# Kernel optimization log

Measured on AMD Instinct MI355X. Metric: run time of the kernel, lower is better.

Reference implementation:

```python
import jax, jax.numpy as jnp
import numpy as np
from jax import lax

B, S, V, E, H, L, LAT = 32, 64, 32000, 128, 512, 2, 64

def setup_inputs() -> dict:
    key = jax.random.key(0)
    ks = jax.random.split(key, 40)
    sc = 0.05
    inputs = jax.random.randint(ks[0], (B, S), 0, V, dtype=jnp.int32)
    lengths = jnp.sort(jax.random.randint(ks[1], (B,), 1, S + 1, dtype=jnp.int32))[::-1]
    lengths = lengths.at[0].set(S)  # enforce_sorted=True, max length == S for static shapes
    d = {
        'inputs': inputs,
        'lengths': lengths,
        'noise': jax.random.normal(ks[2], (L, B, LAT), jnp.float32),
        'embed_table': jax.random.normal(ks[3], (V, E), jnp.float32) * sc,
        'enc_Wm': jax.random.normal(ks[4], (LAT, E), jnp.float32) * sc,
        'enc_bm': jnp.zeros((LAT,), jnp.float32),
        'enc_Wv': jax.random.normal(ks[5], (LAT, E), jnp.float32) * sc,
        'enc_bv': jnp.zeros((LAT,), jnp.float32),
        'W_l2r': jax.random.normal(ks[6], (H, LAT), jnp.float32) * sc,
        'b_l2r': jnp.zeros((H,), jnp.float32),
        'gru_Wih0': jax.random.normal(ks[7], (3 * H, E), jnp.float32) * sc,
        'gru_Whh0': jax.random.normal(ks[8], (3 * H, H), jnp.float32) * sc,
        'gru_bih0': jnp.zeros((3 * H,), jnp.float32),
        'gru_bhh0': jnp.zeros((3 * H,), jnp.float32),
        'gru_Wih1': jax.random.normal(ks[9], (3 * H, H), jnp.float32) * sc,
        'gru_Whh1': jax.random.normal(ks[10], (3 * H, H), jnp.float32) * sc,
        'gru_bih1': jnp.zeros((3 * H,), jnp.float32),
        'gru_bhh1': jnp.zeros((3 * H,), jnp.float32),
        'W_out': jax.random.normal(ks[11], (V, H), jnp.float32) * sc,
        'b_out': jnp.zeros((V,), jnp.float32),
        'logp_W1': jax.random.normal(ks[12], (200, LAT), jnp.float32) * sc,
        'logp_b1': jnp.zeros((200,), jnp.float32),
        'logp_W2': jax.random.normal(ks[13], (100, 200), jnp.float32) * sc,
        'logp_b2': jnp.zeros((100,), jnp.float32),
        'logp_W3': jax.random.normal(ks[14], (1, 100), jnp.float32) * sc,
        'logp_b3': jnp.zeros((1,), jnp.float32),
        'sas_W1': jax.random.normal(ks[15], (200, LAT), jnp.float32) * sc,
        'sas_b1': jnp.zeros((200,), jnp.float32),
        'sas_W2': jax.random.normal(ks[16], (100, 200), jnp.float32) * sc,
        'sas_b2': jnp.zeros((100,), jnp.float32),
        'sas_W3': jax.random.normal(ks[17], (1, 100), jnp.float32) * sc,
        'sas_b3': jnp.zeros((1,), jnp.float32),
    }
    return d

def _gru_layer(x, h0, Wih, Whh, bih, bhh, lengths):
    # x: [B,T,D]; PyTorch GRU gate order: r, z, n. Packed semantics: state frozen
    # and output zero beyond each sample's length.
    T = x.shape[1]
    xW = jnp.einsum('btd,gd->btg', x, Wih) + bih          # [B,T,3H] one big GEMM
    tmask = jnp.arange(T)[:, None] < lengths[None, :]      # [T,B]
    def step(h, inp):
        xw_t, m_t = inp                                    # [B,3H], [B]
        hW = h @ Whh.T + bhh
        xr, xz, xn = jnp.split(xw_t, 3, axis=-1)
        hr, hz, hn = jnp.split(hW, 3, axis=-1)
        r = jax.nn.sigmoid(xr + hr)
        u = jax.nn.sigmoid(xz + hz)
        n = jnp.tanh(xn + r * hn)
        h_new = (1.0 - u) * n + u * h
        m = m_t[:, None]
        h = jnp.where(m, h_new, h)
        out = jnp.where(m, h_new, 0.0)
        return h, out
    hT, outs = lax.scan(step, h0, (xW.transpose(1, 0, 2), tmask))
    return outs.transpose(1, 0, 2), hT                     # [B,T,H], [B,H]

def _mlp3(x, W1, b1, W2, b2, W3, b3):
    h = jax.nn.relu(x @ W1.T + b1)
    h = jax.nn.relu(h @ W2.T + b2)
    return (h @ W3.T + b3).reshape(-1)

def reference(inputs, lengths, noise, embed_table, enc_Wm, enc_bm, enc_Wv, enc_bv,
              W_l2r, b_l2r, gru_Wih0, gru_Whh0, gru_bih0, gru_bhh0,
              gru_Wih1, gru_Whh1, gru_bih1, gru_bhh1, W_out, b_out,
              logp_W1, logp_b1, logp_W2, logp_b2, logp_W3, logp_b3,
              sas_W1, sas_b1, sas_W2, sas_b2, sas_W3, sas_b3):
    emb = embed_table[inputs]                              # [B,S,E] gather
    # ragged masked segment-sum: sum embeddings of tokens with id > 2 per sample
    mask = (inputs > 2)[..., None].astype(emb.dtype)
    vec_frag = jnp.sum(emb * mask, axis=1)                 # [B,E]
    mean = vec_frag @ enc_Wm.T + enc_bm                    # [B,LAT]
    logv = vec_frag @ enc_Wv.T + enc_bv
    std = jnp.exp(0.5 * logv)
    z = noise * std + mean                                 # [L,B,LAT]
    pred_logp = _mlp3(mean, logp_W1, logp_b1, logp_W2, logp_b2, logp_W3, logp_b3)
    pred_sas = _mlp3(mean, sas_W1, sas_b1, sas_W2, sas_b2, sas_W3, sas_b3)
    state = z @ W_l2r.T + b_l2r                            # [L,B,H]
    # decoder: 2-layer GRU (eval mode: no dropout), then vocab projection
    out0, _ = _gru_layer(emb, state[0], gru_Wih0, gru_Whh0, gru_bih0, gru_bhh0, lengths)
    out1, _ = _gru_layer(out0, state[1], gru_Wih1, gru_Whh1, gru_bih1, gru_bhh1, lengths)
    output = out1 @ W_out.T + b_out                        # [B,S,V]
    return (output, mean, std, z, pred_logp, pred_sas)
```

## Files before the change

kernel.cpp:

```cpp
#include <hip/hip_runtime.h>


typedef __attribute__((ext_vector_type(8))) short bf16x8_t;
typedef __attribute__((ext_vector_type(8))) unsigned short u16x8_t;
typedef __attribute__((ext_vector_type(4))) float f32x4_t;
typedef __attribute__((ext_vector_type(8))) _Float16 f16x8_t;
typedef __attribute__((ext_vector_type(4))) unsigned int u32x4_t;

#define AS_AGENT __HIP_MEMORY_SCOPE_AGENT

static __device__ __forceinline__ unsigned short f2bf(float f) {
    unsigned int u = __float_as_uint(f);
    u += 0x7fffu + ((u >> 16) & 1u);
    return (unsigned short)(u >> 16);
}
static __device__ __forceinline__ unsigned short f2h(float f) {
    _Float16 h = (_Float16)f;
    return __builtin_bit_cast(unsigned short, h);
}
static __device__ __forceinline__ float sigmoidf_(float x) {
    return 1.f / (1.f + __expf(-x));
}

__global__ __launch_bounds__(256) void embed_encoder_kernel(
    const int* __restrict__ tok, const float* __restrict__ table,
    const float* __restrict__ Wih0f,
    const float* __restrict__ Wm, const float* __restrict__ bm,
    const float* __restrict__ Wv, const float* __restrict__ bv,
    const float* __restrict__ noise,
    const float* __restrict__ Wl2r, const float* __restrict__ bl2r,
    const float* __restrict__ lW1, const float* __restrict__ lb1,
    const float* __restrict__ lW2, const float* __restrict__ lb2,
    const float* __restrict__ lW3, const float* __restrict__ lb3,
    const float* __restrict__ sW1, const float* __restrict__ sb1,
    const float* __restrict__ sW2, const float* __restrict__ sb2,
    const float* __restrict__ sW3, const float* __restrict__ sb3,
    float* __restrict__ o_mean, float* __restrict__ o_std, float* __restrict__ o_z,
    float* __restrict__ o_logp, float* __restrict__ o_sas,
    float* __restrict__ state,
    unsigned short* __restrict__ embb,
    unsigned short* __restrict__ Wih0b)
{
    const int b = blockIdx.x, tid = threadIdx.x;
    __shared__ float v_[128], mn[64], sd[64], zz[2][64], hh1[200], hh2[100];
    if (tid < 128) {
        const int e = tid;
        float acc = 0.f;
        for (int s = 0; s < 64; ++s) {
            int id = tok[b * 64 + s];
            float v = table[(size_t)id * 128 + e];
            embb[(size_t)(b * 64 + s) * 128 + e] = f2bf(v);
            if (id > 2) acc += v;
        }
        v_[e] = acc;
    }
    for (int i = b * 256 + tid; i < 49152; i += 8192) {
        float4 v = reinterpret_cast<const float4*>(Wih0f)[i];
        ushort4 o;
        o.x = f2bf(v.x); o.y = f2bf(v.y); o.z = f2bf(v.z); o.w = f2bf(v.w);
        reinterpret_cast<ushort4*>(Wih0b)[i] = o;
    }
    __syncthreads();
    if (tid < 128) {
        int j = tid & 63;
        bool isv = tid >= 64;
        const float* W = (isv ? Wv : Wm) + j * 128;
        float a = isv ? bv[j] : bm[j];
#pragma unroll 4
        for (int k = 0; k < 128; ++k) a = fmaf(v_[k], W[k], a);
        if (!isv) { mn[j] = a; o_mean[b * 64 + j] = a; }
        else      { float s = __expf(0.5f * a); sd[j] = s; o_std[b * 64 + j] = s; }
    }
    __syncthreads();
    if (tid < 128) {
        int l = tid >> 6, j = tid & 63;
        float zv = fmaf(noise[(l * 32 + b) * 64 + j], sd[j], mn[j]);
        zz[l][j] = zv;
        o_z[(l * 32 + b) * 64 + j] = zv;
    }
    __syncthreads();
#pragma unroll
    for (int p = 0; p < 4; ++p) {
        int tt = p * 256 + tid;
        int l = tt >> 9, hd = tt & 511;
        const float* W = Wl2r + hd * 64;
        float a = bl2r[hd];
#pragma unroll 4
        for (int k = 0; k < 64; ++k) a = fmaf(zz[l][k], W[k], a);
        state[(size_t)(l * 32 + b) * 512 + hd] = a;
    }
    if (tid < 200) {
        const float* W = lW1 + tid * 64;
        float a = lb1[tid];
        for (int k = 0; k < 64; ++k) a = fmaf(mn[k], W[k], a);
        hh1[tid] = fmaxf(a, 0.f);
    }
    __syncthreads();
    if (tid < 100) {
        const float* W = lW2 + tid * 200;
        float a = lb2[tid];
        for (int k = 0; k < 200; ++k) a = fmaf(hh1[k], W[k], a);
        hh2[tid] = fmaxf(a, 0.f);
    }
    __syncthreads();
    if (tid == 0) {
        float a = lb3[0];
        for (int k = 0; k < 100; ++k) a = fmaf(hh2[k], lW3[k], a);
        o_logp[b] = a;
    }
    __syncthreads();
    if (tid < 200) {
        const float* W = sW1 + tid * 64;
        float a = sb1[tid];
        for (int k = 0; k < 64; ++k) a = fmaf(mn[k], W[k], a);
        hh1[tid] = fmaxf(a, 0.f);
    }
    __syncthreads();
    if (tid < 100) {
        const float* W = sW2 + tid * 200;
        float a = sb2[tid];
        for (int k = 0; k < 200; ++k) a = fmaf(hh1[k], W[k], a);
        hh2[tid] = fmaxf(a, 0.f);
    }
    __syncthreads();
    if (tid == 0) {
        float a = sb3[0];
        for (int k = 0; k < 100; ++k) a = fmaf(hh2[k], sW3[k], a);
        o_sas[b] = a;
    }
}

__global__ __launch_bounds__(256) void gemm_bt_kernel(
    const unsigned short* __restrict__ A,
    const unsigned short* __restrict__ B,
    const float* __restrict__ bias,
    float* __restrict__ C,
    int M, int N, int K)
{
    __shared__ unsigned short lA[128 * 64];
    __shared__ unsigned short lB[128 * 64];
    const int tid = threadIdx.x;
    const int lane = tid & 63;
    const int wave = tid >> 6;
    const int wm = wave >> 1, wn = wave & 1;
    const int m0 = blockIdx.y * 128, n0 = blockIdx.x * 128;

    f32x4_t acc[4][4];
#pragma unroll
    for (int i = 0; i < 4; ++i)
#pragma unroll
        for (int j = 0; j < 4; ++j) acc[i][j] = (f32x4_t){0.f, 0.f, 0.f, 0.f};

    for (int kt = 0; kt < K; kt += 64) {
#pragma unroll
        for (int p = 0; p < 4; ++p) {
            int g = p * 256 + tid;
            int row = g >> 3, c8 = g & 7;
            int dst = row * 64 + ((c8 ^ (row & 7)) << 3);
            *(u16x8_t*)&lA[dst] = *(const u16x8_t*)(A + (size_t)(m0 + row) * K + kt + (c8 << 3));
            *(u16x8_t*)&lB[dst] = *(const u16x8_t*)(B + (size_t)(n0 + row) * K + kt + (c8 << 3));
        }
        __syncthreads();
#pragma unroll
        for (int kc = 0; kc < 2; ++kc) {
            bf16x8_t af[4], bfr[4];
            int c8 = kc * 4 + (lane >> 4);
#pragma unroll
            for (int i = 0; i < 4; ++i) {
                int ra = wm * 64 + i * 16 + (lane & 15);
                af[i] = *(const bf16x8_t*)&lA[ra * 64 + ((c8 ^ (ra & 7)) << 3)];
                int rb = wn * 64 + i * 16 + (lane & 15);
                bfr[i] = *(const bf16x8_t*)&lB[rb * 64 + ((c8 ^ (rb & 7)) << 3)];
            }
#pragma unroll
            for (int i = 0; i < 4; ++i)
#pragma unroll
                for (int j = 0; j < 4; ++j)
                    acc[i][j] = __builtin_amdgcn_mfma_f32_16x16x32_bf16(af[i], bfr[j], acc[i][j], 0, 0, 0);
        }
        __syncthreads();
    }
    const int lm = (lane >> 4) * 4, ln = lane & 15;
#pragma unroll
    for (int i = 0; i < 4; ++i) {
        int gm = m0 + wm * 64 + i * 16 + lm;
#pragma unroll
        for (int j = 0; j < 4; ++j) {
            int gn = n0 + wn * 64 + j * 16 + ln;
            float bb = bias ? bias[gn] : 0.f;
#pragma unroll
            for (int r = 0; r < 4; ++r)
                C[(size_t)(gm + r) * N + gn] = acc[i][j][r] + bb;
        }
    }
}

#define NWG_L0 16
#define NWG_TOT 48
#define NWG_ALL 256
#define NWG_GEMM 208
#define OCH 32832

__global__ __launch_bounds__(512) void gru_fused_kernel(
    const float* __restrict__ xW0,
    const float* __restrict__ Whh0, const float* __restrict__ bhh0,
    const float* __restrict__ Whh1, const float* __restrict__ Wih1,
    const float* __restrict__ bih1, const float* __restrict__ bhh1,
    const float* __restrict__ hinit,
    const int* __restrict__ lengths,
    unsigned short* __restrict__ h0x,
    unsigned short* __restrict__ h1x,
    unsigned short* __restrict__ o0x,
    unsigned short* __restrict__ out1x,
    const float* __restrict__ Woutf,
    unsigned short* __restrict__ Woutb,
    const float* __restrict__ bout,
    float* __restrict__ outp,
    int* __restrict__ flags)
{
    __shared__ __align__(16) char smem[157184];
    const int tid = threadIdx.x;
    const int wg = blockIdx.x;
    const int lane = tid & 63;
    const int wave = tid >> 6;
    unsigned int* __restrict__ h0x32 = (unsigned int*)h0x;
    unsigned int* __restrict__ h1x32 = (unsigned int*)h1x;
    unsigned int* __restrict__ o0x32 = (unsigned int*)o0x;
    unsigned int* __restrict__ o1x32 = (unsigned int*)out1x;

    (void)__hip_atomic_load(&flags[0], __ATOMIC_ACQUIRE, AS_AGENT);

    if (wg >= NWG_TOT) {
        unsigned short* lA = (unsigned short*)smem;
        unsigned short* lB = (unsigned short*)(smem + 16384);
        const int g = wg - NWG_TOT;
        const int wm = wave >> 2;
        const int wn = wave & 3;

        for (int i = g * 512 + tid; i < 4096000; i += NWG_GEMM * 512) {
            float4 v = reinterpret_cast<const float4*>(Woutf)[i];
            unsigned int lo = (unsigned int)f2bf(v.x) | ((unsigned int)f2bf(v.y) << 16);
            unsigned int hi = (unsigned int)f2bf(v.z) | ((unsigned int)f2bf(v.w) << 16);
            unsigned long long w = (unsigned long long)lo | ((unsigned long long)hi << 32);
            __hip_atomic_store((unsigned long long*)Woutb + i, w, __ATOMIC_RELAXED, AS_AGENT);
        }
        asm volatile("s_waitcnt vmcnt(0)" ::: "memory");
        __syncthreads();
        if (tid == 0) __hip_atomic_store(&flags[wg << 5], 1, __ATOMIC_RELAXED, AS_AGENT);
        if (wave == 0) {
            for (;;) {
                int mn = 1;
#pragma unroll
                for (int j = 0; j < 4; ++j) {
                    int idx = lane * 4 + j;
                    if (idx < NWG_GEMM) {
                        int v = __hip_atomic_load(&flags[(NWG_TOT + idx) << 5],
                                                  __ATOMIC_RELAXED, AS_AGENT);
                        mn = v < mn ? v : mn;
                    }
                }
                if (__all(mn >= 1)) break;
                __builtin_amdgcn_s_sleep(8);
            }
        }
        __syncthreads();

        int mPrev = -1;
        for (int T = g; T < 4000; T += NWG_GEMM) {
            const int m = T / 250, n = T % 250;
            if (m != mPrev) {
                if (wave == 0) {
                    const int tgt = 4 * m + 6;
                    for (;;) {
                        int v = 0x40000000;
                        if (lane < 32)
                            v = __hip_atomic_load(&flags[(NWG_L0 + lane) << 5],
                                                  __ATOMIC_RELAXED, AS_AGENT);
                        if (__all(v >= tgt)) break;
                        __builtin_amdgcn_s_sleep(8);
                    }
                }
                __syncthreads();
                mPrev = m;
            }
            f32x4_t acc[4][2];
#pragma unroll
            for (int i = 0; i < 4; ++i)
#pragma unroll
                for (int j = 0; j < 2; ++j) acc[i][j] = (f32x4_t){0.f, 0.f, 0.f, 0.f};

            for (int kt = 0; kt < 512; kt += 64) {
#pragma unroll
                for (int p = 0; p < 2; ++p) {
                    int gi = p * 512 + tid;
                    int row = gi >> 3, c8 = gi & 7;
                    int dst = row * 64 + ((c8 ^ (row & 7)) << 3);
                    u32x4_t qa = *(const u32x4_t*)(out1x + (size_t)m * 65664 +
                                                   row * 512 + kt + (c8 << 3));
                    u32x4_t qb = *(const u32x4_t*)(Woutb + ((size_t)(n * 128 + row)) * 512 +
                                                   kt + (c8 << 3));
                    *(u32x4_t*)&lA[dst] = qa;
                    *(u32x4_t*)&lB[dst] = qb;
                }
                __syncthreads();
#pragma unroll
                for (int kc = 0; kc < 2; ++kc) {
                    bf16x8_t af[4], bfr[2];
                    int c8 = kc * 4 + (lane >> 4);
#pragma unroll
                    for (int i = 0; i < 4; ++i) {
                        int ra = wm * 64 + i * 16 + (lane & 15);
                        af[i] = *(const bf16x8_t*)&lA[ra * 64 + ((c8 ^ (ra & 7)) << 3)];
                    }
#pragma unroll
                    for (int j = 0; j < 2; ++j) {
                        int rb = wn * 32 + j * 16 + (lane & 15);
                        bfr[j] = *(const bf16x8_t*)&lB[rb * 64 + ((c8 ^ (rb & 7)) << 3)];
                    }
#pragma unroll
                    for (int i = 0; i < 4; ++i)
#pragma unroll
                        for (int j = 0; j < 2; ++j)
                            acc[i][j] = __builtin_amdgcn_mfma_f32_16x16x32_bf16(
                                af[i], bfr[j], acc[i][j], 0, 0, 0);
                }
                __syncthreads();
            }
            const int lm = (lane >> 4) * 4, ln = lane & 15;
#pragma unroll
            for (int i = 0; i < 4; ++i) {
                int rl0 = wm * 64 + i * 16 + lm;
#pragma unroll
                for (int j = 0; j < 2; ++j) {
                    int gn = n * 128 + wn * 32 + j * 16 + ln;
                    float bb = bout[gn];
#pragma unroll
                    for (int r = 0; r < 4; ++r) {
                        int rl = rl0 + r;
                        int t = 4 * m + (rl >> 5), b = rl & 31;
                        outp[(size_t)(b * 64 + t) * 32000 + gn] = acc[i][j][r] + bb;
                    }
                }
            }
        }
        return;
    }

    unsigned short* Wl = (unsigned short*)smem;
    u32x4_t* hstage4 = (u32x4_t*)(smem + 98304);
    float* csm = (float*)(smem + 131072);
#define CSM(p, gt, b, c) csm[((((p)*3 + (gt)) * 32 + (b)) * 34) + (c)]
    const int gate = wave >> 1;
    const int mt = wave & 1;

    if (wg < NWG_L0) {
        const int d0 = wg * 32;
        for (int idx = tid; idx < 6144; idx += 512) {
            int ln = idx & 63, kk = (idx >> 6) & 15, nt = (idx >> 10) & 1, g_ = idx >> 11;
            int grow = g_ * 512 + d0 + nt * 16 + (ln & 15);
            int k = kk * 32 + ((ln >> 4) << 3);
            const float* src = Whh0 + (size_t)grow * 512 + k;
            f16x8_t v;
#pragma unroll
            for (int j = 0; j < 8; ++j) v[j] = (_Float16)src[j];
            *(f16x8_t*)&Wl[idx << 3] = v;
        }
        const int ub = tid >> 4, dpl = (tid & 15) * 2, ud = d0 + dpl;
        float h_lo = hinit[(size_t)ub * 512 + ud];
        float h_hi = hinit[(size_t)ub * 512 + ud + 1];
        const float br_lo = bhh0[ud],        br_hi = bhh0[ud + 1];
        const float bz_lo = bhh0[512 + ud],  bz_hi = bhh0[512 + ud + 1];
        const float bn_lo = bhh0[1024 + ud], bn_hi = bhh0[1024 + ud + 1];
        const int lenb = lengths[ub];
        {
            unsigned int hw = (unsigned int)f2h(h_lo) | ((unsigned int)f2h(h_hi) << 16);
            __hip_atomic_store(&h0x32[ub * 256 + (ud >> 1)], hw, __ATOMIC_RELAXED, AS_AGENT);
        }
        asm volatile("s_waitcnt vmcnt(0)" ::: "memory");
        __syncthreads();
        if (tid == 0) __hip_atomic_store(&flags[wg << 5], 1, __ATOMIC_RELAXED, AS_AGENT);
        const float* xrow = xW0 + (size_t)(ub * 64) * 1536 + ud;
        float2 px_r = *(const float2*)(xrow);
        float2 px_z = *(const float2*)(xrow + 512);
        float2 px_n = *(const float2*)(xrow + 1024);

        for (int r = 0; r < 64; ++r) {
            if (wave == 0) {
                const int tgt = r + 1;
                for (;;) {
                    int v = 0x40000000;
                    if (lane < NWG_TOT)
                        v = __hip_atomic_load(&flags[lane << 5], __ATOMIC_RELAXED, AS_AGENT);
                    if (__all(v >= tgt)) break;
                    __builtin_amdgcn_s_sleep(1);
                }
            }
            __syncthreads();
            {
                const char* srcb = (const char*)h0x + ((r & 1) << 15);
                u32x4_t q0, q1, q2, q3;
                asm volatile("global_load_dwordx4 %0, %1, off sc0 sc1"
                             : "=v"(q0) : "v"(srcb + ((size_t)tid << 4)) : "memory");
                asm volatile("global_load_dwordx4 %0, %1, off sc0 sc1"
                             : "=v"(q1) : "v"(srcb + ((size_t)(512 + tid) << 4)) : "memory");
                asm volatile("global_load_dwordx4 %0, %1, off sc0 sc1"
                             : "=v"(q2) : "v"(srcb + ((size_t)(1024 + tid) << 4)) : "memory");
                asm volatile("global_load_dwordx4 %0, %1, off sc0 sc1"
                             : "=v"(q3) : "v"(srcb + ((size_t)(1536 + tid) << 4)) : "memory");
                asm volatile("s_waitcnt vmcnt(0)" ::: "memory");
                int g0 = tid, g1 = 512 + tid, g2 = 1024 + tid, g3 = 1536 + tid;
                hstage4[g0 ^ ((g0 >> 6) & 7)] = q0;
                hstage4[g1 ^ ((g1 >> 6) & 7)] = q1;
                hstage4[g2 ^ ((g2 >> 6) & 7)] = q2;
                hstage4[g3 ^ ((g3 >> 6) & 7)] = q3;
            }
            __syncthreads();
            if (wave < 6) {
                const int brow = mt * 16 + (lane & 15);
                const int ko = lane >> 4;
                f32x4_t acc0 = (f32x4_t){0.f, 0.f, 0.f, 0.f};
                f32x4_t acc1 = (f32x4_t){0.f, 0.f, 0.f, 0.f};
#pragma unroll
                for (int kk = 0; kk < 16; ++kk) {
                    int gg = brow * 64 + kk * 4 + ko;
                    f16x8_t af = __builtin_bit_cast(f16x8_t, hstage4[gg ^ (brow & 7)]);
                    f16x8_t bf0 = *(const f16x8_t*)&Wl[(((gate * 2 + 0) * 16 + kk) * 64 + lane) << 3];
                    f16x8_t bf1 = *(const f16x8_t*)&Wl[(((gate * 2 + 1) * 16 + kk) * 64 + lane) << 3];
                    acc0 = __builtin_amdgcn_mfma_f32_16x16x32_f16(af, bf0, acc0, 0, 0, 0);
                    acc1 = __builtin_amdgcn_mfma_f32_16x16x32_f16(af, bf1, acc1, 0, 0, 0);
                }
                const int crow = mt * 16 + ((lane >> 4) << 2), ccol = lane & 15;
#pragma unroll
                for (int rr = 0; rr < 4; ++rr) {
                    CSM(0, gate, crow + rr, ccol) = acc0[rr];
                    CSM(0, gate, crow + rr, 16 + ccol) = acc1[rr];
                }
            }
            __syncthreads();
            unsigned int ow = 0u;
            if (r < lenb) {
                float hr_lo = CSM(0, 0, ub, dpl), hr_hi = CSM(0, 0, ub, dpl + 1);
                float hz_lo = CSM(0, 1, ub, dpl), hz_hi = CSM(0, 1, ub, dpl + 1);
                float hn_lo = CSM(0, 2, ub, dpl), hn_hi = CSM(0, 2, ub, dpl + 1);
                float r0 = sigmoidf_(px_r.x + hr_lo + br_lo);
                float r1 = sigmoidf_(px_r.y + hr_hi + br_hi);
                float u0 = sigmoidf_(px_z.x + hz_lo + bz_lo);
                float u1 = sigmoidf_(px_z.y + hz_hi + bz_hi);
                float n0 = tanhf(px_n.x + r0 * (hn_lo + bn_lo));
                float n1 = tanhf(px_n.y + r1 * (hn_hi + bn_hi));
                h_lo = (1.f - u0) * n0 + u0 * h_lo;
                h_hi = (1.f - u1) * n1 + u1 * h_hi;
                ow = (unsigned int)f2h(h_lo) | ((unsigned int)f2h(h_hi) << 16);
            }
            {
                unsigned int hw = (unsigned int)f2h(h_lo) | ((unsigned int)f2h(h_hi) << 16);
                __hip_atomic_store(&h0x32[((r + 1) & 1) * 8192 + ub * 256 + (ud >> 1)],
                                   hw, __ATOMIC_RELAXED, AS_AGENT);
                __hip_atomic_store(&o0x32[(r & 1) * 8192 + ub * 256 + (ud >> 1)],
                                   ow, __ATOMIC_RELAXED, AS_AGENT);
            }
            asm volatile("s_waitcnt vmcnt(0)" ::: "memory");
            __syncthreads();
            if (tid == 0) __hip_atomic_store(&flags[wg << 5], r + 2, __ATOMIC_RELAXED, AS_AGENT);
            {
                int tn = r + 1 < 64 ? r + 1 : 63;
                const float* xp = xW0 + (size_t)(ub * 64 + tn) * 1536 + ud;
                px_r = *(const float2*)(xp);
                px_z = *(const float2*)(xp + 512);
                px_n = *(const float2*)(xp + 1024);
            }
        }
    } else {
        const int lid = wg - NWG_L0;
        const int d0 = lid * 16;
        for (int idx = tid; idx < 6144; idx += 512) {
            int ln = idx & 63, kk = (idx >> 6) & 31, g_ = idx >> 11;
            int grow = g_ * 512 + d0 + (ln & 15);
            int k = (kk & 15) * 32 + ((ln >> 4) << 3);
            const float* src = (kk < 16 ? Whh1 : Wih1) + (size_t)grow * 512 + k;
            f16x8_t v;
#pragma unroll
            for (int j = 0; j < 8; ++j) v[j] = (_Float16)src[j];
            *(f16x8_t*)&Wl[idx << 3] = v;
        }
        const bool upd = (tid < 256);
        const int ub = tid >> 3, dpl = (tid & 7) * 2, ud = d0 + dpl;
        float h_lo = 0.f, h_hi = 0.f;
        float br_lo = 0.f, br_hi = 0.f, bz_lo = 0.f, bz_hi = 0.f;
        float bxn_lo = 0.f, bxn_hi = 0.f, bhn_lo = 0.f, bhn_hi = 0.f;
        int lenb = 0;
        if (upd) {
            h_lo = hinit[16384 + (size_t)ub * 512 + ud];
            h_hi = hinit[16384 + (size_t)ub * 512 + ud + 1];
            br_lo = bih1[ud] + bhh1[ud];
            br_hi = bih1[ud + 1] + bhh1[ud + 1];
            bz_lo = bih1[512 + ud] + bhh1[512 + ud];
            bz_hi = bih1[512 + ud + 1] + bhh1[512 + ud + 1];
            bxn_lo = bih1[1024 + ud];   bxn_hi = bih1[1024 + ud + 1];
            bhn_lo = bhh1[1024 + ud];   bhn_hi = bhh1[1024 + ud + 1];
            lenb = lengths[ub];
            unsigned int hw = (unsigned int)f2h(h_lo) | ((unsigned int)f2h(h_hi) << 16);
            __hip_atomic_store(&h1x32[8192 + ub * 256 + (ud >> 1)], hw, __ATOMIC_RELAXED, AS_AGENT);
        }
        asm volatile("s_waitcnt vmcnt(0)" ::: "memory");
        __syncthreads();
        if (tid == 0) __hip_atomic_store(&flags[wg << 5], 2, __ATOMIC_RELAXED, AS_AGENT);

        for (int r = 1; r <= 64; ++r) {
            const int t1 = r - 1;
            if (wave == 0) {
                const int tgt = r + 1;
                for (;;) {
                    int v = 0x40000000;
                    if (lane < NWG_TOT)
                        v = __hip_atomic_load(&flags[lane << 5], __ATOMIC_RELAXED, AS_AGENT);
                    if (__all(v >= tgt)) break;
                    __builtin_amdgcn_s_sleep(1);
                }
            }
            __syncthreads();
            u32x4_t a0, a1, a2, a3, b0, b1, b2, b3;
            {
                const char* sh = (const char*)h1x + ((r & 1) << 15);
                const char* so = (const char*)o0x + (((r + 1) & 1) << 15);
                asm volatile("global_load_dwordx4 %0, %1, off sc0 sc1"
                             : "=v"(a0) : "v"(sh + ((size_t)tid << 4)) : "memory");
                asm volatile("global_load_dwordx4 %0, %1, off sc0 sc1"
                             : "=v"(a1) : "v"(sh + ((size_t)(512 + tid) << 4)) : "memory");
                asm volatile("global_load_dwordx4 %0, %1, off sc0 sc1"
                             : "=v"(a2) : "v"(sh + ((size_t)(1024 + tid) << 4)) : "memory");
                asm volatile("global_load_dwordx4 %0, %1, off sc0 sc1"
                             : "=v"(a3) : "v"(sh + ((size_t)(1536 + tid) << 4)) : "memory");
                asm volatile("global_load_dwordx4 %0, %1, off sc0 sc1"
                             : "=v"(b0) : "v"(so + ((size_t)tid << 4)) : "memory");
                asm volatile("global_load_dwordx4 %0, %1, off sc0 sc1"
                             : "=v"(b1) : "v"(so + ((size_t)(512 + tid) << 4)) : "memory");
                asm volatile("global_load_dwordx4 %0, %1, off sc0 sc1"
                             : "=v"(b2) : "v"(so + ((size_t)(1024 + tid) << 4)) : "memory");
                asm volatile("global_load_dwordx4 %0, %1, off sc0 sc1"
                             : "=v"(b3) : "v"(so + ((size_t)(1536 + tid) << 4)) : "memory");
                asm volatile("s_waitcnt vmcnt(4)" ::: "memory");
                int g0 = tid, g1 = 512 + tid, g2 = 1024 + tid, g3 = 1536 + tid;
                hstage4[g0 ^ ((g0 >> 6) & 7)] = a0;
                hstage4[g1 ^ ((g1 >> 6) & 7)] = a1;
                hstage4[g2 ^ ((g2 >> 6) & 7)] = a2;
                hstage4[g3 ^ ((g3 >> 6) & 7)] = a3;
            }
            __syncthreads();
            f32x4_t acc_h = (f32x4_t){0.f, 0.f, 0.f, 0.f};
            const int brow = mt * 16 + (lane & 15);
            const int ko = lane >> 4;
            if (wave < 6) {
#pragma unroll
                for (int kk = 0; kk < 16; ++kk) {
                    int gg = brow * 64 + kk * 4 + ko;
                    f16x8_t af = __builtin_bit_cast(f16x8_t, hstage4[gg ^ (brow & 7)]);
                    f16x8_t bf = *(const f16x8_t*)&Wl[(((gate * 32 + kk) * 64 + lane)) << 3];
                    acc_h = __builtin_amdgcn_mfma_f32_16x16x32_f16(af, bf, acc_h, 0, 0, 0);
                }
            }
            __syncthreads();
            {
                asm volatile("s_waitcnt vmcnt(0)" ::: "memory");
                int g0 = tid, g1 = 512 + tid, g2 = 1024 + tid, g3 = 1536 + tid;
                hstage4[g0 ^ ((g0 >> 6) & 7)] = b0;
                hstage4[g1 ^ ((g1 >> 6) & 7)] = b1;
                hstage4[g2 ^ ((g2 >> 6) & 7)] = b2;
                hstage4[g3 ^ ((g3 >> 6) & 7)] = b3;
            }
            __syncthreads();
            if (wave < 6) {
                f32x4_t acc_x = (f32x4_t){0.f, 0.f, 0.f, 0.f};
#pragma unroll
                for (int kk = 0; kk < 16; ++kk) {
                    int gg = brow * 64 + kk * 4 + ko;
                    f16x8_t af = __builtin_bit_cast(f16x8_t, hstage4[gg ^ (brow & 7)]);
                    f16x8_t bf = *(const f16x8_t*)&Wl[(((gate * 32 + 16 + kk) * 64 + lane)) << 3];
                    acc_x = __builtin_amdgcn_mfma_f32_16x16x32_f16(af, bf, acc_x, 0, 0, 0);
                }
                const int crow = mt * 16 + ((lane >> 4) << 2), ccol = lane & 15;
#pragma unroll
                for (int rr = 0; rr < 4; ++rr) {
                    CSM(0, gate, crow + rr, ccol) = acc_h[rr];
                    CSM(1, gate, crow + rr, ccol) = acc_x[rr];
                }
            }
            __syncthreads();
            unsigned int ow = 0u;
            if (upd) {
                if (t1 < lenb) {
                    float hr_lo = CSM(0, 0, ub, dpl), hr_hi = CSM(0, 0, ub, dpl + 1);
                    float hz_lo = CSM(0, 1, ub, dpl), hz_hi = CSM(0, 1, ub, dpl + 1);
                    float hn_lo = CSM(0, 2, ub, dpl), hn_hi = CSM(0, 2, ub, dpl + 1);
                    float xr_lo = CSM(1, 0, ub, dpl), xr_hi = CSM(1, 0, ub, dpl + 1);
                    float xz_lo = CSM(1, 1, ub, dpl), xz_hi = CSM(1, 1, ub, dpl + 1);
                    float xn_lo = CSM(1, 2, ub, dpl), xn_hi = CSM(1, 2, ub, dpl + 1);
                    float r0 = sigmoidf_(xr_lo + hr_lo + br_lo);
                    float r1 = sigmoidf_(xr_hi + hr_hi + br_hi);
                    float u0 = sigmoidf_(xz_lo + hz_lo + bz_lo);
                    float u1 = sigmoidf_(xz_hi + hz_hi + bz_hi);
                    float n0 = tanhf(xn_lo + bxn_lo + r0 * (hn_lo + bhn_lo));
                    float n1 = tanhf(xn_hi + bxn_hi + r1 * (hn_hi + bhn_hi));
                    h_lo = (1.f - u0) * n0 + u0 * h_lo;
                    h_hi = (1.f - u1) * n1 + u1 * h_hi;
                    ow = (unsigned int)f2bf(h_lo) | ((unsigned int)f2bf(h_hi) << 16);
                }
                if (r < 64) {
                    unsigned int hw = (unsigned int)f2h(h_lo) | ((unsigned int)f2h(h_hi) << 16);
                    __hip_atomic_store(&h1x32[((r + 1) & 1) * 8192 + ub * 256 + (ud >> 1)],
                                       hw, __ATOMIC_RELAXED, AS_AGENT);
                }
                __hip_atomic_store(&o1x32[(size_t)(t1 >> 2) * OCH +
                                          ((t1 & 3) * 32 + ub) * 256 + (ud >> 1)],
                                   ow, __ATOMIC_RELAXED, AS_AGENT);
            }
            asm volatile("s_waitcnt vmcnt(0)" ::: "memory");
            __syncthreads();
            if (tid == 0)
                __hip_atomic_store(&flags[wg << 5], r + 2, __ATOMIC_RELAXED, AS_AGENT);
        }
    }
#undef CSM
}

extern "C" void kernel_launch(void* const* d_in, const int* in_sizes, int n_in,
                              void* d_out, int out_size, void* d_ws, size_t ws_size,
                              hipStream_t stream) {
    const int*   tok    = (const int*)d_in[0];
    const int*   lens   = (const int*)d_in[1];
    const float* noise  = (const float*)d_in[2];
    const float* table  = (const float*)d_in[3];
    const float* Wm     = (const float*)d_in[4];
    const float* bm_    = (const float*)d_in[5];
    const float* Wv     = (const float*)d_in[6];
    const float* bv_    = (const float*)d_in[7];
    const float* Wl2r   = (const float*)d_in[8];
    const float* bl2r   = (const float*)d_in[9];
    const float* Wih0   = (const float*)d_in[10];
    const float* Whh0   = (const float*)d_in[11];
    const float* bih0   = (const float*)d_in[12];
    const float* bhh0   = (const float*)d_in[13];
    const float* Wih1   = (const float*)d_in[14];
    const float* Whh1   = (const float*)d_in[15];
    const float* bih1   = (const float*)d_in[16];
    const float* bhh1   = (const float*)d_in[17];
    const float* Wout   = (const float*)d_in[18];
    const float* bout   = (const float*)d_in[19];
    const float* lW1 = (const float*)d_in[20]; const float* lb1 = (const float*)d_in[21];
    const float* lW2 = (const float*)d_in[22]; const float* lb2 = (const float*)d_in[23];
    const float* lW3 = (const float*)d_in[24]; const float* lb3 = (const float*)d_in[25];
    const float* sW1 = (const float*)d_in[26]; const float* sb1 = (const float*)d_in[27];
    const float* sW2 = (const float*)d_in[28]; const float* sb2 = (const float*)d_in[29];
    const float* sW3 = (const float*)d_in[30]; const float* sb3 = (const float*)d_in[31];

    float* out    = (float*)d_out;
    float* o_mean = out + 65536000;
    float* o_std  = o_mean + 2048;
    float* o_z    = o_std + 2048;
    float* o_logp = o_z + 4096;
    float* o_sas  = o_logp + 32;

    char* ws = (char*)d_ws;
    unsigned short* Woutb = (unsigned short*)ws;  ws += 32768000;
    unsigned short* Wih0b = (unsigned short*)ws;  ws += 393216;
    unsigned short* embb  = (unsigned short*)ws;  ws += 524288;
    float*          state = (float*)ws;           ws += 131072;
    float*          xW    = (float*)ws;           ws += 12582912;
    unsigned short* out1x = (unsigned short*)ws;  ws += 2101248;
    unsigned short* h0x   = (unsigned short*)ws;  ws += 131072;
    unsigned short* h1x   = (unsigned short*)ws;  ws += 131072;
    unsigned short* o0x   = (unsigned short*)ws;  ws += 131072;
    int*            flgp  = (int*)ws;             ws += 32768;

    (void)hipMemsetAsync(flgp, 0, 32768, stream);

    embed_encoder_kernel<<<dim3(32), dim3(256), 0, stream>>>(
        tok, table, Wih0, Wm, bm_, Wv, bv_, noise, Wl2r, bl2r,
        lW1, lb1, lW2, lb2, lW3, lb3, sW1, sb1, sW2, sb2, sW3, sb3,
        o_mean, o_std, o_z, o_logp, o_sas, state, embb, Wih0b);

    gemm_bt_kernel<<<dim3(12, 16), dim3(256), 0, stream>>>(embb, Wih0b, bih0, xW, 2048, 1536, 128);
    gru_fused_kernel<<<dim3(NWG_ALL), dim3(512), 0, stream>>>(
        xW, Whh0, bhh0, Whh1, Wih1, bih1, bhh1, state, lens,
        h0x, h1x, o0x, out1x, Wout, Woutb, bout, out, flgp);
}
```

Measured before the change: 380.2 us.

## Replace global Wout conversion barrier with per-panel ready flags and nontemporal accesses

```diff
diff --git a/kernel.cpp b/kernel.cpp
--- a/kernel.cpp
+++ b/kernel.cpp
@@ -11,6 +11,10 @@
 
 static __device__ __forceinline__ unsigned short f2bf(float f) {
     unsigned int u = __float_as_uint(f);
+    u += 0x7fffu + ((u >> 16) & 1u);
+    return (unsigned short)(u >> 16);
+}
+static __device__ __forceinline__ unsigned short bfround(unsigned int u) {
     u += 0x7fffu + ((u >> 16) & 1u);
     return (unsigned short)(u >> 16);
 }
@@ -237,33 +241,21 @@
         const int wm = wave >> 2;
         const int wn = wave & 3;
 
-        for (int i = g * 512 + tid; i < 4096000; i += NWG_GEMM * 512) {
-            float4 v = reinterpret_cast<const float4*>(Woutf)[i];
-            unsigned int lo = (unsigned int)f2bf(v.x) | ((unsigned int)f2bf(v.y) << 16);
-            unsigned int hi = (unsigned int)f2bf(v.z) | ((unsigned int)f2bf(v.w) << 16);
-            unsigned long long w = (unsigned long long)lo | ((unsigned long long)hi << 32);
-            __hip_atomic_store((unsigned long long*)Woutb + i, w, __ATOMIC_RELAXED, AS_AGENT);
-        }
-        asm volatile("s_waitcnt vmcnt(0)" ::: "memory");
-        __syncthreads();
-        if (tid == 0) __hip_atomic_store(&flags[wg << 5], 1, __ATOMIC_RELAXED, AS_AGENT);
-        if (wave == 0) {
-            for (;;) {
-                int mn = 1;
-#pragma unroll
-                for (int j = 0; j < 4; ++j) {
-                    int idx = lane * 4 + j;
-                    if (idx < NWG_GEMM) {
-                        int v = __hip_atomic_load(&flags[(NWG_TOT + idx) << 5],
-                                                  __ATOMIC_RELAXED, AS_AGENT);
-                        mn = v < mn ? v : mn;
-                    }
-                }
-                if (__all(mn >= 1)) break;
-                __builtin_amdgcn_s_sleep(8);
-            }
-        }
-        __syncthreads();
+        for (int pn = g; pn < 250; pn += NWG_GEMM) {
+            const u32x4_t* src = (const u32x4_t*)Woutf + (size_t)pn * 16384;
+            unsigned long long* dst = (unsigned long long*)Woutb + (size_t)pn * 16384;
+            for (int i = tid; i < 16384; i += 512) {
+                u32x4_t q = __builtin_nontemporal_load(src + i);
+                unsigned int lo = (unsigned int)bfround(q[0]) | ((unsigned int)bfround(q[1]) << 16);
+                unsigned int hi = (unsigned int)bfround(q[2]) | ((unsigned int)bfround(q[3]) << 16);
+                unsigned long long w = (unsigned long long)lo | ((unsigned long long)hi << 32);
+                __hip_atomic_store(dst + i, w, __ATOMIC_RELAXED, AS_AGENT);
+            }
+            asm volatile("s_waitcnt vmcnt(0)" ::: "memory");
+            __syncthreads();
+            if (tid == 0)
+                __hip_atomic_store(&flags[2048 + pn * 16], 1, __ATOMIC_RELAXED, AS_AGENT);
+        }
 
         int mPrev = -1;
         for (int T = g; T < 4000; T += NWG_GEMM) {
@@ -280,9 +272,14 @@
                         __builtin_amdgcn_s_sleep(8);
                     }
                 }
-                __syncthreads();
                 mPrev = m;
             }
+            if (wave == 0) {
+                while (__hip_atomic_load(&flags[2048 + n * 16], __ATOMIC_RELAXED, AS_AGENT) < 1)
+                    __builtin_amdgcn_s_sleep(8);
+            }
+            __syncthreads();
+
             f32x4_t acc[4][2];
 #pragma unroll
             for (int i = 0; i < 4; ++i)
@@ -338,7 +335,8 @@
                     for (int r = 0; r < 4; ++r) {
                         int rl = rl0 + r;
                         int t = 4 * m + (rl >> 5), b = rl & 31;
-                        outp[(size_t)(b * 64 + t) * 32000 + gn] = acc[i][j][r] + bb;
+                        __builtin_nontemporal_store(acc[i][j][r] + bb,
+                            &outp[(size_t)(b * 64 + t) * 32000 + gn]);
                     }
                 }
             }
```

New measurement: 354.5 us. 6.8% less time.
